# Performance work log

Hardware: AMD Instinct MI355X
Metric: run time of the kernel (lower is better)

Reference implementation:

```python
import jax, jax.numpy as jnp
import numpy as np

# Matches the torch constant: 1/sqrt(2*3.14159) (NOT math.pi)
INV_SQRT_2PI = 1.0 / np.sqrt(np.float32(2.0 * 3.14159))


def density_ir_normal(x):
    return INV_SQRT_2PI * jnp.exp(-0.5 * x * x)


def setup_inputs() -> dict:
    key = jax.random.key(0)
    k1, k2, k3 = jax.random.split(key, 3)
    batch = 8388608           # 2**23 output slots
    n_events = 16777216       # 2**24 scattered events (avg 2 per slot)
    idx = jax.random.randint(k1, (n_events,), 0, batch)
    vals = jax.random.normal(k2, (n_events,), dtype=jnp.float32)
    # theta0 in (0,1) (branch prob), theta1 > 0 (scale), theta2 (loc)
    thetas = jnp.array([0.7, 1.3, 0.2], dtype=jnp.float32)
    return {"batch": batch, "idx": idx, "vals": vals, "thetas": thetas}


def reference(batch, idx, vals, thetas):
    # l_4_high = min(thetas[0], 1); l_5 = max(l_4_high, 0) -> clip(theta0, 0, 1)
    l_5_lhs_integral = jnp.clip(thetas[0], 0.0, 1.0)
    l_1_cond = 1.0 - l_5_lhs_integral
    # per-event multiplicative factor (vectorized density evaluation)
    z = (vals - thetas[2]) / thetas[1]
    factors = (1.0 - l_1_cond) * density_ir_normal(z) / thetas[1]
    # multiplicative scatter; duplicate indices multiply in (matches the
    # sequential result[idx[i]] *= factor loop, product is order-invariant)
    result = jnp.ones(batch, dtype=vals.dtype).at[idx].multiply(factors)
    return result * l_1_cond
```

## Files before the change

### kernel.cpp

```cpp
#include <hip/hip_runtime.h>
#include <climits>


#define INV_SQRT_2PI 0.39894246f
#define SLOT_BITS 14
#define SLOTS (1 << SLOT_BITS)
#define NB_MAX 512
#define NBLK 512
#define BTHREADS 512
#define TILE 4096
#define RING 32
#define QSCALE 8192.0f
#define QMASK 0x3FFFFu

#define LDS_BAR() do {                                        \
    asm volatile("s_waitcnt lgkmcnt(0)" ::: "memory");        \
    __builtin_amdgcn_s_barrier();                             \
} while (0)

__device__ __forceinline__ long long region_idx(int blk, int b, int nbuckets,
                                                int swzmask) {
    int bb = swzmask ? ((b + blk) & swzmask) : b;
    return (long long)blk * nbuckets + bb;
}

__device__ __forceinline__ int ring_slot(int b, int pos) {
    return b * RING + ((pos & (RING - 1)) ^ ((b & 7) << 2));
}

__device__ __forceinline__ void ovf_push(uint2* ovf, int* ovf_cnt, int ovcap,
                                         unsigned gslot, unsigned q) {
    int op = atomicAdd(ovf_cnt, 1);
    if (op < ovcap) ovf[op] = make_uint2(gslot, q);
}

__global__ __launch_bounds__(BTHREADS) void bin_kernel(
        const int* __restrict__ idx, const float* __restrict__ vals,
        const float* __restrict__ thetas,
        unsigned* __restrict__ pairs,
        int* __restrict__ fill,
        uint2* __restrict__ ovf, int* __restrict__ ovf_cnt, int ovcap,
        int n, int nbuckets, int cap_shift, int swzmask, int epb) {
    __shared__ unsigned ring[NB_MAX * RING];
    __shared__ int scnt[NB_MAX];
    __shared__ int cnum[NB_MAX];

    const int tid = threadIdx.x;
    const int blk = blockIdx.x;
    const int cappb = 1 << cap_shift;
    long long start = (long long)blk * epb;
    long long end = start + epb;
    if (end > n) end = n;

    for (int b = tid; b < nbuckets; b += BTHREADS) { scnt[b] = 0; cnum[b] = 0; }
    __syncthreads();

    const float t1 = thetas[1], t2 = thetas[2];
    const float t0c = fminf(fmaxf(thetas[0], 0.0f), 1.0f);
    const float inv_t1 = 1.0f / t1;

    int   kk[8]; float vv[8]; int cnt_ev = 0;
    int   nk[8]; float nv[8];
    {
        long long te0 = start + TILE; if (te0 > end) te0 = end;
        long long base = start + (long long)tid * 8;
        if (base + 8 <= te0) {
            int4 k0 = *(const int4*)(idx + base);
            int4 k1 = *(const int4*)(idx + base + 4);
            float4 v0 = *(const float4*)(vals + base);
            float4 v1 = *(const float4*)(vals + base + 4);
            kk[0]=k0.x;kk[1]=k0.y;kk[2]=k0.z;kk[3]=k0.w;
            kk[4]=k1.x;kk[5]=k1.y;kk[6]=k1.z;kk[7]=k1.w;
            vv[0]=v0.x;vv[1]=v0.y;vv[2]=v0.z;vv[3]=v0.w;
            vv[4]=v1.x;vv[5]=v1.y;vv[6]=v1.z;vv[7]=v1.w;
            cnt_ev = 8;
        } else if (base < te0) {
            cnt_ev = (int)(te0 - base);
            #pragma unroll
            for (int i = 0; i < 8; ++i) { kk[i] = 0; vv[i] = 0.0f; }
            for (int i = 0; i < cnt_ev; ++i) { kk[i] = idx[base+i]; vv[i] = vals[base+i]; }
        }
    }

    for (long long ts = start; ts < end; ts += TILE) {
        int nxt_cnt = 0;
        long long tsn = ts + TILE;
        if (tsn < end) {
            long long ten = tsn + TILE; if (ten > end) ten = end;
            long long base = tsn + (long long)tid * 8;
            if (base + 8 <= ten) {
                int4 k0 = *(const int4*)(idx + base);
                int4 k1 = *(const int4*)(idx + base + 4);
                float4 v0 = *(const float4*)(vals + base);
                float4 v1 = *(const float4*)(vals + base + 4);
                nk[0]=k0.x;nk[1]=k0.y;nk[2]=k0.z;nk[3]=k0.w;
                nk[4]=k1.x;nk[5]=k1.y;nk[6]=k1.z;nk[7]=k1.w;
                nv[0]=v0.x;nv[1]=v0.y;nv[2]=v0.z;nv[3]=v0.w;
                nv[4]=v1.x;nv[5]=v1.y;nv[6]=v1.z;nv[7]=v1.w;
                nxt_cnt = 8;
            } else if (base < ten) {
                nxt_cnt = (int)(ten - base);
                #pragma unroll
                for (int i = 0; i < 8; ++i) { nk[i] = 0; nv[i] = 0.0f; }
                for (int i = 0; i < nxt_cnt; ++i) { nk[i] = idx[base+i]; nv[i] = vals[base+i]; }
            }
        }

        int bs[8]; unsigned recs[8]; int pos[8]; int win[8];
        #pragma unroll
        for (int j = 0; j < 8; ++j) {
            unsigned uk = (unsigned)kk[j];
            bs[j] = (int)(uk >> SLOT_BITS);
            float z = (vv[j] - t2) * inv_t1;
            float u = 0.5f * z * z;
            unsigned q = __float2uint_rn(fminf(u * QSCALE, (float)QMASK));
            recs[j] = ((uk & (SLOTS - 1)) << 18) | q;
        }
        #pragma unroll
        for (int j = 0; j < 8; ++j) {
            bool ok = (j < cnt_ev) && (bs[j] < nbuckets);
            win[j] = ok ? (cnum[bs[j]] << 4) : 0;
            pos[j] = ok ? atomicAdd(&scnt[bs[j]], 1) : INT_MAX;
        }
        #pragma unroll
        for (int j = 0; j < 8; ++j) {
            if (pos[j] == INT_MAX) continue;
            if (pos[j] - win[j] < RING)
                ring[ring_slot(bs[j], pos[j])] = recs[j];
            else
                ovf_push(ovf, ovf_cnt, ovcap, (unsigned)kk[j], recs[j] & QMASK);
        }
        LDS_BAR();

        for (int b = tid; b < nbuckets; b += BTHREADS) {
            int c = scnt[b];
            int J = cnum[b];
            int flushed = J << 4;
            int stored_end = c < flushed + RING ? c : flushed + RING;
            int navail = stored_end - flushed;
            while (navail >= 16) {
                int H = (J & 1) ^ ((b >> 2) & 1);
                const uint4* s4 = (const uint4*)&ring[b * RING + (H << 4)];
                if (J < (cappb >> 4)) {
                    uint4* d4 = (uint4*)(pairs +
                        (region_idx(blk, b, nbuckets, swzmask) << cap_shift) + (J << 4));
                    d4[0]=s4[0]; d4[1]=s4[1]; d4[2]=s4[2]; d4[3]=s4[3];
                } else {
                    for (int i = 0; i < 16; ++i) {
                        unsigned r = ring[b * RING + (H << 4) + i];
                        ovf_push(ovf, ovf_cnt, ovcap,
                                 ((unsigned)b << SLOT_BITS) | (r >> 18), r & QMASK);
                    }
                }
                ++J; flushed += 16; navail -= 16;
            }
            cnum[b] = J;
            if (c != stored_end) scnt[b] = stored_end;
        }
        LDS_BAR();

        cnt_ev = nxt_cnt;
        #pragma unroll
        for (int j = 0; j < 8; ++j) { kk[j] = nk[j]; vv[j] = nv[j]; }
    }

    for (int b = tid; b < nbuckets; b += BTHREADS) {
        int c = scnt[b];
        int J = cnum[b];
        int flushed = J << 4;
        int r = c - flushed;
        int valid = flushed;
        if (r > 0 && J < (cappb >> 4)) {
            unsigned tmp[16];
            int lbase = (J & 1) << 4;
            #pragma unroll
            for (int i = 0; i < 16; ++i)
                tmp[i] = ring[b * RING + ((lbase + i) ^ ((b & 7) << 2))];
            uint4* d4 = (uint4*)(pairs +
                (region_idx(blk, b, nbuckets, swzmask) << cap_shift) + (J << 4));
            const uint4* t4 = (const uint4*)tmp;
            d4[0]=t4[0]; d4[1]=t4[1]; d4[2]=t4[2]; d4[3]=t4[3];
            valid = flushed + r;
        } else if (r > 0) {
            int lbase = (J & 1) << 4;
            for (int i = 0; i < r; ++i) {
                unsigned rr = ring[b * RING + ((lbase + i) ^ ((b & 7) << 2))];
                ovf_push(ovf, ovf_cnt, ovcap,
                         ((unsigned)b << SLOT_BITS) | (rr >> 18), rr & QMASK);
            }
        }
        fill[region_idx(blk, b, nbuckets, swzmask)] = valid;
    }
}

__global__ __launch_bounds__(1024) void reduce_kernel(
        const unsigned* __restrict__ pairs, const int* __restrict__ fill,
        const uint2* __restrict__ ovf, const int* __restrict__ ovf_cnt, int ovcap,
        const float* __restrict__ thetas, float* __restrict__ out,
        long long n_out, int nbuckets, int cap_shift, int swzmask) {
    __shared__ unsigned accu[SLOTS];
    const int tid = threadIdx.x;
    const int b = blockIdx.x;

    for (int s = tid; s < SLOTS; s += 1024) accu[s] = 0u;
    __syncthreads();

    const int wave = tid >> 6, lane = tid & 63;
    const int SEGS = NBLK / 16;

    int sl = wave + (lane & 31) * 16;
    int cntv = fill[region_idx(sl, b, nbuckets, swzmask)];

    const unsigned* pc = pairs +
        (region_idx(wave, b, nbuckets, swzmask) << cap_shift);
    unsigned a0 = pc[lane];
    unsigned a1 = pc[64 + lane];

    for (int i = 0; i < SEGS; ++i) {
        const unsigned* pn = pc; unsigned n0 = 0, n1 = 0;
        if (i < SEGS - 1) {
            int sn = wave + (i + 1) * 16;
            pn = pairs + (region_idx(sn, b, nbuckets, swzmask) << cap_shift);
            n0 = pn[lane];
            n1 = pn[64 + lane];
        }
        int ca = __builtin_amdgcn_readlane(cntv, i);
        if (lane < ca)      atomicAdd(&accu[a0 >> 18], (1u << 25) + (a0 & QMASK));
        if (64 + lane < ca) atomicAdd(&accu[a1 >> 18], (1u << 25) + (a1 & QMASK));
        for (int r = 128 + lane; r < ca; r += 64) {
            unsigned rec = pc[r];
            atomicAdd(&accu[rec >> 18], (1u << 25) + (rec & QMASK));
        }
        pc = pn; a0 = n0; a1 = n1;
    }
    __syncthreads();

    int no = *ovf_cnt; if (no > ovcap) no = ovcap;
    for (int i = tid; i < no; i += 1024) {
        uint2 e = ovf[i];
        if ((int)(e.x >> SLOT_BITS) == b)
            atomicAdd(&accu[e.x & (SLOTS - 1)], (1u << 25) + e.y);
    }
    __syncthreads();

    const float t1 = thetas[1];
    const float t0c = fminf(fmaxf(thetas[0], 0.0f), 1.0f);
    const float logC = logf(t0c * INV_SQRT_2PI / t1);
    const float cond = 1.0f - t0c;
    long long obase = (long long)b << SLOT_BITS;
    for (int ss = tid; ss < SLOTS; ss += 1024) {
        long long o = obase + ss;
        if (o < n_out) {
            unsigned av = accu[ss];
            float v = (float)(av >> 25) * logC
                    - (float)(av & 0x1FFFFFFu) * (1.0f / QSCALE);
            out[o] = cond * expf(v);
        }
    }
}

__global__ void init_zero_kernel(float* __restrict__ out, int n) {
    int i = blockIdx.x * blockDim.x + threadIdx.x;
    int stride = gridDim.x * blockDim.x;
    for (; i < n; i += stride) out[i] = 0.0f;
}
__global__ void scatter_log_kernel(const int* __restrict__ idx,
                                   const float* __restrict__ vals,
                                   const float* __restrict__ thetas,
                                   float* __restrict__ acc, int n) {
    float t1 = thetas[1], t2 = thetas[2];
    float t0c = fminf(fmaxf(thetas[0], 0.0f), 1.0f);
    float logC = logf(t0c * INV_SQRT_2PI / t1);
    float inv_t1 = 1.0f / t1;
    int i = blockIdx.x * blockDim.x + threadIdx.x;
    int stride = gridDim.x * blockDim.x;
    for (; i < n; i += stride) {
        float z = (vals[i] - t2) * inv_t1;
        atomicAdd(&acc[idx[i]], fmaf(-0.5f * z, z, logC));
    }
}
__global__ void finalize_kernel(float* __restrict__ out,
                                const float* __restrict__ thetas, int n) {
    float t0c = fminf(fmaxf(thetas[0], 0.0f), 1.0f);
    float cond = 1.0f - t0c;
    int i = blockIdx.x * blockDim.x + threadIdx.x;
    int stride = gridDim.x * blockDim.x;
    for (; i < n; i += stride) out[i] = cond * expf(out[i]);
}

extern "C" void kernel_launch(void* const* d_in, const int* in_sizes, int n_in,
                              void* d_out, int out_size, void* d_ws, size_t ws_size,
                              hipStream_t stream) {
    const int*   idx    = (const int*)d_in[1];
    const float* vals   = (const float*)d_in[2];
    const float* thetas = (const float*)d_in[3];
    float*       out    = (float*)d_out;

    int n_events = in_sizes[1];
    long long n_out = out_size;
    int nbuckets = (int)((n_out + SLOTS - 1) >> SLOT_BITS);

    long long tiles_total = ((long long)n_events + TILE - 1) / TILE;
    long long tpb = (tiles_total + NBLK - 1) / NBLK;
    int epb = (int)(tpb * TILE);
    long long avg = nbuckets > 0 ? (epb + nbuckets - 1) / nbuckets : 1;
    long long want = avg + avg / 2 + 32;
    int cap_shift = 6;
    while ((1LL << cap_shift) < want && cap_shift < 20) ++cap_shift;
    long long cappb = 1LL << cap_shift;
    int swzmask = (nbuckets > 0 && (nbuckets & (nbuckets - 1)) == 0)
                  ? nbuckets - 1 : 0;

    size_t pairs_b = (size_t)NBLK * nbuckets * cappb * 4;
    size_t fill_b  = (size_t)NBLK * nbuckets * 4;
    size_t head    = pairs_b + fill_b + 64;
    bool fast = (nbuckets > 0) && (nbuckets <= NB_MAX) && (n_events > 0) &&
                (ws_size >= head + 64 * 1024);

    if (fast) {
        unsigned* pairs = (unsigned*)d_ws;
        int* fill = (int*)((char*)d_ws + pairs_b);
        int* ovf_cnt = (int*)((char*)d_ws + pairs_b + fill_b);
        uint2* ovf = (uint2*)((char*)d_ws + head);
        long long ovcap_ll = (long long)((ws_size - head) / 8);
        int ovcap = (int)(ovcap_ll > 4194304 ? 4194304 : ovcap_ll);

        hipMemsetAsync(ovf_cnt, 0, sizeof(int), stream);
        bin_kernel<<<NBLK, BTHREADS, 0, stream>>>(idx, vals, thetas, pairs, fill,
                                                  ovf, ovf_cnt, ovcap,
                                                  n_events, nbuckets, cap_shift,
                                                  swzmask, epb);
        reduce_kernel<<<nbuckets, 1024, 0, stream>>>(pairs, fill, ovf, ovf_cnt,
                                                     ovcap, thetas, out,
                                                     n_out, nbuckets, cap_shift,
                                                     swzmask);
    } else {
        const int BLOCK = 256;
        int grid_out = min((int)((n_out + BLOCK - 1) / BLOCK), 2048);
        int grid_ev  = min((n_events + BLOCK - 1) / BLOCK, 2048);
        init_zero_kernel<<<grid_out, BLOCK, 0, stream>>>(out, (int)n_out);
        scatter_log_kernel<<<grid_ev, BLOCK, 0, stream>>>(idx, vals, thetas, out, n_events);
        finalize_kernel<<<grid_out, BLOCK, 0, stream>>>(out, thetas, (int)n_out);
    }
}
```

Baseline: 98.48 us.

## Pack flush counter into bucket count and transpose LDS ring layout

Doubles bin-kernel threads to 1024, so each thread handles 4 events per tile instead of 8. It merges the per-bucket flush counter (cnum) into the high bits of scnt, so one LDS atomicAdd returns both the position and the flushed-chunk index, removing a separate LDS read per event. The ring is transposed to slot-major [pos][bucket] layout, and flush reads gather 16 strided words into registers before storing. The strided gather may cost more LDS instructions during flush. The added `fast` condition term is a no-op comma expression.

```diff
diff --git a/kernel.cpp b/kernel.cpp
--- a/kernel.cpp
+++ b/kernel.cpp
@@ -7,11 +7,12 @@
 #define SLOTS (1 << SLOT_BITS)
 #define NB_MAX 512
 #define NBLK 512
-#define BTHREADS 512
+#define BTHREADS 1024
 #define TILE 4096
 #define RING 32
 #define QSCALE 8192.0f
 #define QMASK 0x3FFFFu
+#define CMASK 0xFFFFFu
 
 #define LDS_BAR() do {                                        \
     asm volatile("s_waitcnt lgkmcnt(0)" ::: "memory");        \
@@ -22,10 +23,6 @@
                                                 int swzmask) {
     int bb = swzmask ? ((b + blk) & swzmask) : b;
     return (long long)blk * nbuckets + bb;
-}
-
-__device__ __forceinline__ int ring_slot(int b, int pos) {
-    return b * RING + ((pos & (RING - 1)) ^ ((b & 7) << 2));
 }
 
 __device__ __forceinline__ void ovf_push(uint2* ovf, int* ovf_cnt, int ovcap,
@@ -41,9 +38,8 @@
         int* __restrict__ fill,
         uint2* __restrict__ ovf, int* __restrict__ ovf_cnt, int ovcap,
         int n, int nbuckets, int cap_shift, int swzmask, int epb) {
-    __shared__ unsigned ring[NB_MAX * RING];
+    __shared__ unsigned ring[RING * NB_MAX];
     __shared__ int scnt[NB_MAX];
-    __shared__ int cnum[NB_MAX];
 
     const int tid = threadIdx.x;
     const int blk = blockIdx.x;
@@ -52,63 +48,55 @@
     long long end = start + epb;
     if (end > n) end = n;
 
-    for (int b = tid; b < nbuckets; b += BTHREADS) { scnt[b] = 0; cnum[b] = 0; }
+    for (int b = tid; b < nbuckets; b += BTHREADS) scnt[b] = 0;
     __syncthreads();
 
     const float t1 = thetas[1], t2 = thetas[2];
     const float t0c = fminf(fmaxf(thetas[0], 0.0f), 1.0f);
     const float inv_t1 = 1.0f / t1;
 
-    int   kk[8]; float vv[8]; int cnt_ev = 0;
-    int   nk[8]; float nv[8];
+    int4 ck = make_int4(0,0,0,0); float4 cv = make_float4(0,0,0,0); int ccnt = 0;
+    int4 pk_; float4 pv_;
     {
         long long te0 = start + TILE; if (te0 > end) te0 = end;
-        long long base = start + (long long)tid * 8;
-        if (base + 8 <= te0) {
-            int4 k0 = *(const int4*)(idx + base);
-            int4 k1 = *(const int4*)(idx + base + 4);
-            float4 v0 = *(const float4*)(vals + base);
-            float4 v1 = *(const float4*)(vals + base + 4);
-            kk[0]=k0.x;kk[1]=k0.y;kk[2]=k0.z;kk[3]=k0.w;
-            kk[4]=k1.x;kk[5]=k1.y;kk[6]=k1.z;kk[7]=k1.w;
-            vv[0]=v0.x;vv[1]=v0.y;vv[2]=v0.z;vv[3]=v0.w;
-            vv[4]=v1.x;vv[5]=v1.y;vv[6]=v1.z;vv[7]=v1.w;
-            cnt_ev = 8;
+        long long base = start + (long long)tid * 4;
+        if (base + 4 <= te0) {
+            ck = *(const int4*)(idx + base);
+            cv = *(const float4*)(vals + base);
+            ccnt = 4;
         } else if (base < te0) {
-            cnt_ev = (int)(te0 - base);
-            #pragma unroll
-            for (int i = 0; i < 8; ++i) { kk[i] = 0; vv[i] = 0.0f; }
-            for (int i = 0; i < cnt_ev; ++i) { kk[i] = idx[base+i]; vv[i] = vals[base+i]; }
+            ccnt = (int)(te0 - base);
+            int kk[4] = {0,0,0,0}; float vv[4] = {0,0,0,0};
+            for (int i = 0; i < ccnt; ++i) { kk[i]=idx[base+i]; vv[i]=vals[base+i]; }
+            ck = make_int4(kk[0],kk[1],kk[2],kk[3]);
+            cv = make_float4(vv[0],vv[1],vv[2],vv[3]);
         }
     }
 
     for (long long ts = start; ts < end; ts += TILE) {
-        int nxt_cnt = 0;
+        int ncnt = 0;
         long long tsn = ts + TILE;
         if (tsn < end) {
             long long ten = tsn + TILE; if (ten > end) ten = end;
-            long long base = tsn + (long long)tid * 8;
-            if (base + 8 <= ten) {
-                int4 k0 = *(const int4*)(idx + base);
-                int4 k1 = *(const int4*)(idx + base + 4);
-                float4 v0 = *(const float4*)(vals + base);
-                float4 v1 = *(const float4*)(vals + base + 4);
-                nk[0]=k0.x;nk[1]=k0.y;nk[2]=k0.z;nk[3]=k0.w;
-                nk[4]=k1.x;nk[5]=k1.y;nk[6]=k1.z;nk[7]=k1.w;
-                nv[0]=v0.x;nv[1]=v0.y;nv[2]=v0.z;nv[3]=v0.w;
-                nv[4]=v1.x;nv[5]=v1.y;nv[6]=v1.z;nv[7]=v1.w;
-                nxt_cnt = 8;
+            long long base = tsn + (long long)tid * 4;
+            if (base + 4 <= ten) {
+                pk_ = *(const int4*)(idx + base);
+                pv_ = *(const float4*)(vals + base);
+                ncnt = 4;
             } else if (base < ten) {
-                nxt_cnt = (int)(ten - base);
-                #pragma unroll
-                for (int i = 0; i < 8; ++i) { nk[i] = 0; nv[i] = 0.0f; }
-                for (int i = 0; i < nxt_cnt; ++i) { nk[i] = idx[base+i]; nv[i] = vals[base+i]; }
+                ncnt = (int)(ten - base);
+                int kk[4] = {0,0,0,0}; float vv[4] = {0,0,0,0};
+                for (int i = 0; i < ncnt; ++i) { kk[i]=idx[base+i]; vv[i]=vals[base+i]; }
+                pk_ = make_int4(kk[0],kk[1],kk[2],kk[3]);
+                pv_ = make_float4(vv[0],vv[1],vv[2],vv[3]);
             }
         }
 
-        int bs[8]; unsigned recs[8]; int pos[8]; int win[8];
+        int   kk[4] = {ck.x, ck.y, ck.z, ck.w};
+        float vv[4] = {cv.x, cv.y, cv.z, cv.w};
+        int bs[4]; unsigned recs[4];
         #pragma unroll
-        for (int j = 0; j < 8; ++j) {
+        for (int j = 0; j < 4; ++j) {
             unsigned uk = (unsigned)kk[j];
             bs[j] = (int)(uk >> SLOT_BITS);
             float z = (vv[j] - t2) * inv_t1;
@@ -116,75 +104,81 @@
             unsigned q = __float2uint_rn(fminf(u * QSCALE, (float)QMASK));
             recs[j] = ((uk & (SLOTS - 1)) << 18) | q;
         }
+        int ret[4];
         #pragma unroll
-        for (int j = 0; j < 8; ++j) {
-            bool ok = (j < cnt_ev) && (bs[j] < nbuckets);
-            win[j] = ok ? (cnum[bs[j]] << 4) : 0;
-            pos[j] = ok ? atomicAdd(&scnt[bs[j]], 1) : INT_MAX;
+        for (int j = 0; j < 4; ++j) {
+            ret[j] = (j < ccnt && bs[j] < nbuckets)
+                     ? atomicAdd(&scnt[bs[j]], 1) : INT_MIN;
         }
         #pragma unroll
-        for (int j = 0; j < 8; ++j) {
-            if (pos[j] == INT_MAX) continue;
-            if (pos[j] - win[j] < RING)
-                ring[ring_slot(bs[j], pos[j])] = recs[j];
+        for (int j = 0; j < 4; ++j) {
+            if (ret[j] == INT_MIN) continue;
+            int pos = ret[j] & CMASK;
+            int fl  = (ret[j] >> 20) << 4;
+            if (pos - fl < RING)
+                ring[(pos & (RING - 1)) * nbuckets + bs[j]] = recs[j];
             else
                 ovf_push(ovf, ovf_cnt, ovcap, (unsigned)kk[j], recs[j] & QMASK);
         }
         LDS_BAR();
 
         for (int b = tid; b < nbuckets; b += BTHREADS) {
-            int c = scnt[b];
-            int J = cnum[b];
-            int flushed = J << 4;
-            int stored_end = c < flushed + RING ? c : flushed + RING;
-            int navail = stored_end - flushed;
-            while (navail >= 16) {
-                int H = (J & 1) ^ ((b >> 2) & 1);
-                const uint4* s4 = (const uint4*)&ring[b * RING + (H << 4)];
+            int pk = scnt[b];
+            int c = pk & CMASK;
+            int J = pk >> 20;
+            int fl = J << 4;
+            int se = c < fl + RING ? c : fl + RING;
+            int na = se - fl;
+            int J0 = J;
+            while (na >= 16) {
+                int H = (J & 1) << 4;
+                unsigned tmp[16];
+                #pragma unroll
+                for (int i = 0; i < 16; ++i)
+                    tmp[i] = ring[(H + i) * nbuckets + b];
                 if (J < (cappb >> 4)) {
                     uint4* d4 = (uint4*)(pairs +
                         (region_idx(blk, b, nbuckets, swzmask) << cap_shift) + (J << 4));
-                    d4[0]=s4[0]; d4[1]=s4[1]; d4[2]=s4[2]; d4[3]=s4[3];
+                    const uint4* t4 = (const uint4*)tmp;
+                    d4[0]=t4[0]; d4[1]=t4[1]; d4[2]=t4[2]; d4[3]=t4[3];
                 } else {
                     for (int i = 0; i < 16; ++i) {
-                        unsigned r = ring[b * RING + (H << 4) + i];
+                        unsigned r = tmp[i];
                         ovf_push(ovf, ovf_cnt, ovcap,
                                  ((unsigned)b << SLOT_BITS) | (r >> 18), r & QMASK);
                     }
                 }
-                ++J; flushed += 16; navail -= 16;
+                ++J; fl += 16; na -= 16;
             }
-            cnum[b] = J;
-            if (c != stored_end) scnt[b] = stored_end;
+            if (J != J0 || se != c) scnt[b] = (J << 20) | se;
         }
         LDS_BAR();
 
-        cnt_ev = nxt_cnt;
-        #pragma unroll
-        for (int j = 0; j < 8; ++j) { kk[j] = nk[j]; vv[j] = nv[j]; }
+        ck = pk_; cv = pv_; ccnt = ncnt;
     }
 
     for (int b = tid; b < nbuckets; b += BTHREADS) {
-        int c = scnt[b];
-        int J = cnum[b];
-        int flushed = J << 4;
-        int r = c - flushed;
-        int valid = flushed;
+        int pk = scnt[b];
+        int c = pk & CMASK;
+        int J = pk >> 20;
+        int fl = J << 4;
+        int r = c - fl;
+        int valid = fl;
         if (r > 0 && J < (cappb >> 4)) {
+            int H = (J & 1) << 4;
             unsigned tmp[16];
-            int lbase = (J & 1) << 4;
             #pragma unroll
             for (int i = 0; i < 16; ++i)
-                tmp[i] = ring[b * RING + ((lbase + i) ^ ((b & 7) << 2))];
+                tmp[i] = ring[(H + i) * nbuckets + b];
             uint4* d4 = (uint4*)(pairs +
                 (region_idx(blk, b, nbuckets, swzmask) << cap_shift) + (J << 4));
             const uint4* t4 = (const uint4*)tmp;
             d4[0]=t4[0]; d4[1]=t4[1]; d4[2]=t4[2]; d4[3]=t4[3];
-            valid = flushed + r;
+            valid = fl + r;
         } else if (r > 0) {
-            int lbase = (J & 1) << 4;
+            int H = (J & 1) << 4;
             for (int i = 0; i < r; ++i) {
-                unsigned rr = ring[b * RING + ((lbase + i) ^ ((b & 7) << 2))];
+                unsigned rr = ring[(H + i) * nbuckets + b];
                 ovf_push(ovf, ovf_cnt, ovcap,
                          ((unsigned)b << SLOT_BITS) | (rr >> 18), rr & QMASK);
             }
@@ -315,7 +309,8 @@
     size_t fill_b  = (size_t)NBLK * nbuckets * 4;
     size_t head    = pairs_b + fill_b + 64;
     bool fast = (nbuckets > 0) && (nbuckets <= NB_MAX) && (n_events > 0) &&
-                (ws_size >= head + 64 * 1024);
+                (ws_size >= head + 64 * 1024) &&
+                ((long long)NBLK * 2048  , true);
 
     if (fast) {
         unsigned* pairs = (unsigned*)d_ws;
```

Result: faster. 96.43 us (-2.1%).
